# Optimization experiments

Hardware: AMD Instinct MI355X
Metric: run time of the kernel (lower is better)

## Reference

```python
import jax, jax.numpy as jnp
import numpy as np

N = 100000      # nodes
E = 1600000     # edges
IN, H, OUT = 128, 128, 64
FUSION_W = 0.5


def setup_inputs() -> dict:
    key = jax.random.key(0)
    ks = jax.random.split(key, 10)
    x = jax.random.normal(ks[0], (N, IN), dtype=jnp.float32)
    edge_index = jax.random.randint(ks[1], (2, E), 0, N, dtype=jnp.int32)

    def lin(k, fi, fo):
        return jax.random.normal(k, (fi, fo), dtype=jnp.float32) / np.float32(np.sqrt(fi))

    return {
        "x": x,
        "edge_index": edge_index,
        "gnn_W1": lin(ks[2], IN, H),  "gnn_b1": jnp.zeros((H,), jnp.float32),
        "gnn_W2": lin(ks[3], H, OUT), "gnn_b2": jnp.zeros((OUT,), jnp.float32),
        "mlp_W1": lin(ks[4], IN, H),  "mlp_b1": jnp.zeros((H,), jnp.float32),
        "mlp_W2": lin(ks[5], H, OUT), "mlp_b2": jnp.zeros((OUT,), jnp.float32),
    }


def _gcn_conv(x, W, b, src, dst, deg_inv_sqrt, deg_inv):
    # GCNConv: x' = D^{-1/2} (A + I) D^{-1/2} (x W) + b, deg counts self-loops
    h = x @ W                                     # [N, F_out]
    norm = deg_inv_sqrt[src] * deg_inv_sqrt[dst]  # [E]
    agg = jax.ops.segment_sum(h[src] * norm[:, None], dst, num_segments=N)
    # self-loop contribution has norm 1/deg
    return agg + h * deg_inv[:, None] + b


def reference(x, edge_index, gnn_W1, gnn_b1, gnn_W2, gnn_b2,
              mlp_W1, mlp_b1, mlp_W2, mlp_b2):
    src, dst = edge_index[0], edge_index[1]
    # in-degree including self-loops (PyG GCNConv default add_self_loops=True)
    deg = 1.0 + jax.ops.segment_sum(jnp.ones((E,), jnp.float32), dst, num_segments=N)
    deg_inv_sqrt = jax.lax.rsqrt(deg)
    deg_inv = 1.0 / deg

    # GNN branch (dropout is identity in eval mode)
    h = jax.nn.relu(_gcn_conv(x, gnn_W1, gnn_b1, src, dst, deg_inv_sqrt, deg_inv))
    z_gnn = _gcn_conv(h, gnn_W2, gnn_b2, src, dst, deg_inv_sqrt, deg_inv)

    # MLP branch
    z_mlp = jax.nn.relu(x @ mlp_W1 + mlp_b1) @ mlp_W2 + mlp_b2

    return FUSION_W * z_gnn + (1.0 - FUSION_W) * z_mlp
```

## Files before the change

### kernel.cpp

```cpp
#include <hip/hip_runtime.h>
#include <hip/hip_fp16.h>

static constexpr int IN_F = 128;
static constexpr int FCAP = 6144;

typedef _Float16 half8 __attribute__((ext_vector_type(8)));
typedef _Float16 half4 __attribute__((ext_vector_type(4)));
typedef float f32x4 __attribute__((ext_vector_type(4)));
typedef float f32x2 __attribute__((ext_vector_type(2)));

__device__ inline void fp8x8_to_f32(uint2 u, float* f) {
    f32x2 a0 = __builtin_amdgcn_cvt_pk_f32_fp8(u.x, false);
    f32x2 a1 = __builtin_amdgcn_cvt_pk_f32_fp8(u.x, true);
    f32x2 a2 = __builtin_amdgcn_cvt_pk_f32_fp8(u.y, false);
    f32x2 a3 = __builtin_amdgcn_cvt_pk_f32_fp8(u.y, true);
    f[0] = a0[0]; f[1] = a0[1]; f[2] = a1[0]; f[3] = a1[1];
    f[4] = a2[0]; f[5] = a2[1]; f[6] = a3[0]; f[7] = a3[1];
}
__device__ inline void fp8x4_to_f32(unsigned u, float* f) {
    f32x2 a0 = __builtin_amdgcn_cvt_pk_f32_fp8(u, false);
    f32x2 a1 = __builtin_amdgcn_cvt_pk_f32_fp8(u, true);
    f[0] = a0[0]; f[1] = a0[1]; f[2] = a1[0]; f[3] = a1[1];
}
__device__ inline unsigned char f32_to_fp8(float v) {
    return (unsigned char)__builtin_amdgcn_cvt_pk_fp8_f32(v, v, 0, false);
}


__global__ __launch_bounds__(1024) void kb_count(const int* __restrict__ dst,
                                                 int* __restrict__ bcount, int E) {
    __shared__ int cnt[512];
    const int tid = threadIdx.x;
    if (tid < 512) cnt[tid] = 0;
    __syncthreads();
#pragma unroll
    for (int q = 0; q < 8; ++q) {
        int i = blockIdx.x * 8192 + q * 1024 + tid;
        if (i < E) atomicAdd(&cnt[dst[i] >> 8], 1);
    }
    __syncthreads();
    if (tid < 512 && cnt[tid] > 0) atomicAdd(&bcount[tid], cnt[tid]);
}

__global__ __launch_bounds__(512) void k_scanb(const int* __restrict__ bcount,
                                               int* __restrict__ bbase,
                                               int* __restrict__ bcursor, int NB) {
    __shared__ int s[512];
    const int tid = threadIdx.x;
    int v = (tid < NB) ? bcount[tid] : 0;
    s[tid] = v;
    __syncthreads();
    int inc = v;
#pragma unroll
    for (int off = 1; off < 512; off <<= 1) {
        int add = (tid >= off) ? s[tid - off] : 0;
        __syncthreads();
        s[tid] = inc = inc + add;
        __syncthreads();
    }
    if (tid < NB) { bbase[tid] = inc - v; bcursor[tid] = inc - v; }
    if (tid == NB - 1) bbase[NB] = inc;
}

__global__ __launch_bounds__(1024) void kb_move(const int* __restrict__ src,
                                                const int* __restrict__ dst,
                                                int* __restrict__ bcursor,
                                                unsigned* __restrict__ recs, int E) {
    __shared__ int cnt[512];
    __shared__ int off[512];
    const int tid = threadIdx.x;
    if (tid < 512) cnt[tid] = 0;
    __syncthreads();

    int bq[8];
    unsigned rq[8];
#pragma unroll
    for (int q = 0; q < 8; ++q) {
        int i = blockIdx.x * 8192 + q * 1024 + tid;
        if (i < E) {
            int d = dst[i];
            int s = src[i];
            bq[q] = d >> 8;
            rq[q] = (unsigned)(((d & 255) << 17) | s);
            atomicAdd(&cnt[bq[q]], 1);
        } else {
            bq[q] = -1;
            rq[q] = 0u;
        }
    }
    __syncthreads();
    if (tid < 512 && cnt[tid] > 0) off[tid] = atomicAdd(&bcursor[tid], cnt[tid]);
    __syncthreads();
#pragma unroll
    for (int q = 0; q < 8; ++q) {
        if (bq[q] >= 0) {
            int p = atomicAdd(&off[bq[q]], 1);
            recs[p] = rq[q];
        }
    }
}

__global__ __launch_bounds__(256) void kb_fill_lds(const unsigned* __restrict__ recs,
                                                   const int* __restrict__ bbase,
                                                   int* __restrict__ row_ptr,
                                                   float* __restrict__ dis,
                                                   int* __restrict__ csr, int n) {
    __shared__ int hist[256];
    __shared__ int sc[256];
    __shared__ int base[257];
    __shared__ int cur[256];
    __shared__ int stage[FCAP];
    const int tid   = threadIdx.x;
    const int b     = blockIdx.x;
    const int s     = bbase[b], e = bbase[b + 1];
    const int nbase = b << 8;

    hist[tid] = 0;
    __syncthreads();
    for (int i = s + tid; i < e; i += 256)
        atomicAdd(&hist[recs[i] >> 17], 1);
    __syncthreads();

    const int v = hist[tid];
    sc[tid] = v;
    __syncthreads();
    int inc = v;
#pragma unroll
    for (int off = 1; off < 256; off <<= 1) {
        int add = (tid >= off) ? sc[tid - off] : 0;
        __syncthreads();
        sc[tid] = inc = inc + add;
        __syncthreads();
    }
    const int excl = inc - v;
    base[tid] = excl;
    if (tid == 255) base[256] = inc;
    cur[tid] = 0;

    const int idx = nbase + tid;
    if (idx < n) {
        row_ptr[idx] = s + excl;
        dis[idx] = rsqrtf(1.0f + (float)v);
    }
    if (idx == n) row_ptr[n] = s + excl;
    if (tid == 255 && nbase + 256 == n) row_ptr[n] = s + inc;
    __syncthreads();

    for (int i = s + tid; i < e; i += 256) {
        unsigned r = recs[i];
        int dl = (int)(r >> 17);
        int slot = base[dl] + atomicAdd(&cur[dl], 1);
        int sr = (int)(r & 0x1FFFFu);
        if (slot < FCAP) stage[slot] = sr;
        else csr[s + slot] = sr;
    }
    __syncthreads();

    const int total = e - s;
    const int lim = total < FCAP ? total : FCAP;
    for (int i = tid; i < lim; i += 256)
        csr[s + i] = stage[i];
}

__global__ __launch_bounds__(256) void k_prep_w(const float* __restrict__ gW1,
                                                const float* __restrict__ mW1,
                                                const float* __restrict__ mW2,
                                                const float* __restrict__ gW2,
                                                _Float16* __restrict__ tg1,
                                                _Float16* __restrict__ tm1,
                                                _Float16* __restrict__ tm2,
                                                _Float16* __restrict__ tg2) {
    int i = blockIdx.x * 256 + threadIdx.x;
    if (i < 16384)      { int j = i;         int f = j >> 7, k = j & 127; tg1[j] = (_Float16)gW1[k * 128 + f]; }
    else if (i < 32768) { int j = i - 16384; int f = j >> 7, k = j & 127; tm1[j] = (_Float16)mW1[k * 128 + f]; }
    else if (i < 40960) { int j = i - 32768; int f = j >> 7, k = j & 127; tm2[j] = (_Float16)mW2[k * 64 + f]; }
    else if (i < 49152) { int j = i - 40960; int f = j >> 7, k = j & 127; tg2[j] = (_Float16)gW2[k * 64 + f]; }
}

__global__ __launch_bounds__(256) void k_dual_mfma(const float* __restrict__ x,
                                                   const _Float16* __restrict__ tg1,
                                                   const _Float16* __restrict__ tm1,
                                                   const _Float16* __restrict__ tm2,
                                                   const float* __restrict__ b1,
                                                   const float* __restrict__ b2,
                                                   const float* __restrict__ dis,
                                                   unsigned char* __restrict__ h1,
                                                   _Float16* __restrict__ z, int nrows) {
    __shared__ _Float16 As[64 * 128];
    __shared__ _Float16 Ws[128 * 128];
    _Float16* Ms = As;
    const int tid  = threadIdx.x;
    const int row0 = blockIdx.x * 64;

#pragma unroll
    for (int p = 0; p < 4; ++p) {
        int sid = p * 256 + tid;
        int r = sid >> 4, s = sid & 15;
        int gr = row0 + r;
        uint4 v = make_uint4(0, 0, 0, 0);
        if (gr < nrows) {
            const float4 f0 = *reinterpret_cast<const float4*>(x + (size_t)gr * 128 + s * 8);
            const float4 f1 = *reinterpret_cast<const float4*>(x + (size_t)gr * 128 + s * 8 + 4);
            _Float16 t[8] = {(_Float16)f0.x, (_Float16)f0.y, (_Float16)f0.z, (_Float16)f0.w,
                             (_Float16)f1.x, (_Float16)f1.y, (_Float16)f1.z, (_Float16)f1.w};
            v = *reinterpret_cast<uint4*>(t);
        }
        *reinterpret_cast<uint4*>(&As[r * 128 + ((s ^ (r & 7)) * 8)]) = v;
    }
#pragma unroll
    for (int p = 0; p < 8; ++p) {
        int sid = p * 256 + tid;
        int r = sid >> 4, s = sid & 15;
        uint4 v = *reinterpret_cast<const uint4*>(tg1 + (size_t)r * 128 + s * 8);
        *reinterpret_cast<uint4*>(&Ws[r * 128 + ((s ^ (r & 7)) * 8)]) = v;
    }
    __syncthreads();

    const int lane = tid & 63;
    const int wv   = tid >> 6;
    const int mrow = wv * 16 + (lane & 15);
    const int kg   = lane >> 4;
    const int grow = row0 + wv * 16 + kg * 4;

    half8 a[4];
#pragma unroll
    for (int kk = 0; kk < 4; ++kk)
        a[kk] = *reinterpret_cast<const half8*>(&As[mrow * 128 + (((kk * 4 + kg) ^ (mrow & 7)) * 8)]);

    float dvals[4];
#pragma unroll
    for (int j = 0; j < 4; ++j)
        dvals[j] = (grow + j < nrows) ? dis[grow + j] : 0.f;

#pragma unroll
    for (int ct = 0; ct < 8; ++ct) {
        const int ncol = ct * 16 + (lane & 15);
        f32x4 acc = {0.f, 0.f, 0.f, 0.f};
#pragma unroll
        for (int kk = 0; kk < 4; ++kk) {
            half8 b = *reinterpret_cast<const half8*>(&Ws[ncol * 128 + (((kk * 4 + kg) ^ (ncol & 7)) * 8)]);
            acc = __builtin_amdgcn_mfma_f32_16x16x32_f16(a[kk], b, acc, 0, 0, 0);
        }
#pragma unroll
        for (int j = 0; j < 4; ++j)
            if (grow + j < nrows)
                h1[(size_t)(grow + j) * 128 + ncol] = f32_to_fp8(acc[j] * dvals[j]);
    }
    __syncthreads();

#pragma unroll
    for (int p = 0; p < 8; ++p) {
        int sid = p * 256 + tid;
        int r = sid >> 4, s = sid & 15;
        uint4 v = *reinterpret_cast<const uint4*>(tm1 + (size_t)r * 128 + s * 8);
        *reinterpret_cast<uint4*>(&Ws[r * 128 + ((s ^ (r & 7)) * 8)]) = v;
    }
    __syncthreads();

#pragma unroll
    for (int ct = 0; ct < 8; ++ct) {
        const int ncol = ct * 16 + (lane & 15);
        f32x4 acc = {0.f, 0.f, 0.f, 0.f};
#pragma unroll
        for (int kk = 0; kk < 4; ++kk) {
            half8 b = *reinterpret_cast<const half8*>(&Ws[ncol * 128 + (((kk * 4 + kg) ^ (ncol & 7)) * 8)]);
            acc = __builtin_amdgcn_mfma_f32_16x16x32_f16(a[kk], b, acc, 0, 0, 0);
        }
        const float bias = b1[ncol];
#pragma unroll
        for (int j = 0; j < 4; ++j) {
            int r = wv * 16 + kg * 4 + j;
            float v = fmaxf((float)acc[j] + bias, 0.f);
            Ms[r * 128 + (((ncol >> 3) ^ (r & 7)) * 8) + (ncol & 7)] = (_Float16)v;
        }
    }
    __syncthreads();

#pragma unroll
    for (int p = 0; p < 4; ++p) {
        int sid = p * 256 + tid;
        int r = sid >> 4, s = sid & 15;
        uint4 v = *reinterpret_cast<const uint4*>(tm2 + (size_t)r * 128 + s * 8);
        *reinterpret_cast<uint4*>(&Ws[r * 128 + ((s ^ (r & 7)) * 8)]) = v;
    }
    __syncthreads();

    half8 am[4];
#pragma unroll
    for (int kk = 0; kk < 4; ++kk)
        am[kk] = *reinterpret_cast<const half8*>(&Ms[mrow * 128 + (((kk * 4 + kg) ^ (mrow & 7)) * 8)]);

#pragma unroll
    for (int ct = 0; ct < 4; ++ct) {
        const int ncol = ct * 16 + (lane & 15);
        f32x4 acc = {0.f, 0.f, 0.f, 0.f};
#pragma unroll
        for (int kk = 0; kk < 4; ++kk) {
            half8 b = *reinterpret_cast<const half8*>(&Ws[ncol * 128 + (((kk * 4 + kg) ^ (ncol & 7)) * 8)]);
            acc = __builtin_amdgcn_mfma_f32_16x16x32_f16(am[kk], b, acc, 0, 0, 0);
        }
        const float bias = b2[ncol];
#pragma unroll
        for (int j = 0; j < 4; ++j)
            if (grow + j < nrows)
                z[(size_t)(grow + j) * 64 + ncol] = (_Float16)((float)acc[j] + bias);
    }
}

__global__ __launch_bounds__(256) void k_mm64(const _Float16* __restrict__ A,
                                              const _Float16* __restrict__ Wt,
                                              const float* __restrict__ dis,
                                              unsigned char* __restrict__ C, int nrows) {
    __shared__ _Float16 As[64 * 128];
    __shared__ _Float16 Ws[64 * 128];
    const int tid  = threadIdx.x;
    const int row0 = blockIdx.x * 64;

#pragma unroll
    for (int p = 0; p < 4; ++p) {
        int sid = p * 256 + tid;
        int r = sid >> 4, s = sid & 15;
        int gr = row0 + r;
        uint4 v = make_uint4(0, 0, 0, 0);
        if (gr < nrows) v = *reinterpret_cast<const uint4*>(A + (size_t)gr * 128 + s * 8);
        *reinterpret_cast<uint4*>(&As[r * 128 + ((s ^ (r & 7)) * 8)]) = v;
    }
#pragma unroll
    for (int p = 0; p < 4; ++p) {
        int sid = p * 256 + tid;
        int r = sid >> 4, s = sid & 15;
        uint4 v = *reinterpret_cast<const uint4*>(Wt + (size_t)r * 128 + s * 8);
        *reinterpret_cast<uint4*>(&Ws[r * 128 + ((s ^ (r & 7)) * 8)]) = v;
    }
    __syncthreads();

    const int lane = tid & 63;
    const int wv   = tid >> 6;
    const int mrow = wv * 16 + (lane & 15);
    const int kg   = lane >> 4;
    const int grow = row0 + wv * 16 + kg * 4;

    half8 a[4];
#pragma unroll
    for (int kk = 0; kk < 4; ++kk)
        a[kk] = *reinterpret_cast<const half8*>(&As[mrow * 128 + (((kk * 4 + kg) ^ (mrow & 7)) * 8)]);

    float dvals[4];
#pragma unroll
    for (int j = 0; j < 4; ++j)
        dvals[j] = (grow + j < nrows) ? dis[grow + j] : 0.f;

#pragma unroll
    for (int ct = 0; ct < 4; ++ct) {
        const int ncol = ct * 16 + (lane & 15);
        f32x4 acc = {0.f, 0.f, 0.f, 0.f};
#pragma unroll
        for (int kk = 0; kk < 4; ++kk) {
            half8 b = *reinterpret_cast<const half8*>(&Ws[ncol * 128 + (((kk * 4 + kg) ^ (ncol & 7)) * 8)]);
            acc = __builtin_amdgcn_mfma_f32_16x16x32_f16(a[kk], b, acc, 0, 0, 0);
        }
#pragma unroll
        for (int j = 0; j < 4; ++j)
            if (grow + j < nrows)
                C[(size_t)(grow + j) * 64 + ncol] = f32_to_fp8(acc[j] * dvals[j]);
    }
}

__global__ __launch_bounds__(256) void k_agg1(const int* __restrict__ rp,
                                              const int* __restrict__ csr,
                                              const float* __restrict__ dis,
                                              const unsigned char* __restrict__ h1,
                                              const float* __restrict__ b,
                                              _Float16* __restrict__ out, int n) {
    const int tid  = threadIdx.x;
    const int node = blockIdx.x * 4 + (tid >> 6);
    if (node >= n) return;
    const int lane = tid & 63;
    const int g    = lane >> 4;
    const int c0   = (lane & 15) * 8;
    const int start = rp[node], end = rp[node + 1];

    float acc[8];
#pragma unroll
    for (int k = 0; k < 8; ++k) acc[k] = 0.f;

    int j = start + g;
    for (; j + 12 < end; j += 16) {
        int s0 = csr[j];
        int s1 = csr[j + 4];
        int s2 = csr[j + 8];
        int s3 = csr[j + 12];
        uint2 u0 = *reinterpret_cast<const uint2*>(h1 + (size_t)s0 * 128 + c0);
        uint2 u1 = *reinterpret_cast<const uint2*>(h1 + (size_t)s1 * 128 + c0);
        uint2 u2 = *reinterpret_cast<const uint2*>(h1 + (size_t)s2 * 128 + c0);
        uint2 u3 = *reinterpret_cast<const uint2*>(h1 + (size_t)s3 * 128 + c0);
        float f0[8], f1[8], f2[8], f3[8];
        fp8x8_to_f32(u0, f0);
        fp8x8_to_f32(u1, f1);
        fp8x8_to_f32(u2, f2);
        fp8x8_to_f32(u3, f3);
#pragma unroll
        for (int k = 0; k < 8; ++k)
            acc[k] += (f0[k] + f1[k]) + (f2[k] + f3[k]);
    }
    for (; j < end; j += 4) {
        int s0 = csr[j];
        uint2 u0 = *reinterpret_cast<const uint2*>(h1 + (size_t)s0 * 128 + c0);
        float f0[8];
        fp8x8_to_f32(u0, f0);
#pragma unroll
        for (int k = 0; k < 8; ++k) acc[k] += f0[k];
    }

#pragma unroll
    for (int k = 0; k < 8; ++k) {
        acc[k] += __shfl_xor(acc[k], 16);
        acc[k] += __shfl_xor(acc[k], 32);
    }

    if (g == 0) {
        const float dd = dis[node];
        uint2 un = *reinterpret_cast<const uint2*>(h1 + (size_t)node * 128 + c0);
        float fn[8];
        fp8x8_to_f32(un, fn);
        const float4 bv0 = *reinterpret_cast<const float4*>(b + c0);
        const float4 bv1 = *reinterpret_cast<const float4*>(b + c0 + 4);
        const float bb[8] = {bv0.x, bv0.y, bv0.z, bv0.w, bv1.x, bv1.y, bv1.z, bv1.w};
        half8 o;
#pragma unroll
        for (int k = 0; k < 8; ++k)
            o[k] = (_Float16)fmaxf(dd * (acc[k] + fn[k]) + bb[k], 0.f);
        *reinterpret_cast<half8*>(out + (size_t)node * 128 + c0) = o;
    }
}

__global__ __launch_bounds__(256) void k_agg2(const int* __restrict__ rp,
                                              const int* __restrict__ csr,
                                              const float* __restrict__ dis,
                                              const unsigned char* __restrict__ h2,
                                              const float* __restrict__ b,
                                              const _Float16* __restrict__ zmlp,
                                              float* __restrict__ out, int n) {
    const int tid  = threadIdx.x;
    const int node = blockIdx.x * 4 + (tid >> 6);
    if (node >= n) return;
    const int lane = tid & 63;
    const int g    = lane >> 4;
    const int c0   = (lane & 15) * 4;
    const int start = rp[node], end = rp[node + 1];

    float acc[4];
#pragma unroll
    for (int k = 0; k < 4; ++k) acc[k] = 0.f;

    int j = start + g;
    for (; j + 12 < end; j += 16) {
        int s0 = csr[j];
        int s1 = csr[j + 4];
        int s2 = csr[j + 8];
        int s3 = csr[j + 12];
        unsigned u0 = *reinterpret_cast<const unsigned*>(h2 + (size_t)s0 * 64 + c0);
        unsigned u1 = *reinterpret_cast<const unsigned*>(h2 + (size_t)s1 * 64 + c0);
        unsigned u2 = *reinterpret_cast<const unsigned*>(h2 + (size_t)s2 * 64 + c0);
        unsigned u3 = *reinterpret_cast<const unsigned*>(h2 + (size_t)s3 * 64 + c0);
        float f0[4], f1[4], f2[4], f3[4];
        fp8x4_to_f32(u0, f0);
        fp8x4_to_f32(u1, f1);
        fp8x4_to_f32(u2, f2);
        fp8x4_to_f32(u3, f3);
#pragma unroll
        for (int k = 0; k < 4; ++k)
            acc[k] += (f0[k] + f1[k]) + (f2[k] + f3[k]);
    }
    for (; j < end; j += 4) {
        int s0 = csr[j];
        unsigned u0 = *reinterpret_cast<const unsigned*>(h2 + (size_t)s0 * 64 + c0);
        float f0[4];
        fp8x4_to_f32(u0, f0);
#pragma unroll
        for (int k = 0; k < 4; ++k) acc[k] += f0[k];
    }

#pragma unroll
    for (int k = 0; k < 4; ++k) {
        acc[k] += __shfl_xor(acc[k], 16);
        acc[k] += __shfl_xor(acc[k], 32);
    }

    if (g == 0) {
        const float dd = dis[node];
        unsigned un = *reinterpret_cast<const unsigned*>(h2 + (size_t)node * 64 + c0);
        float fn[4];
        fp8x4_to_f32(un, fn);
        half4 zm = *reinterpret_cast<const half4*>(zmlp + (size_t)node * 64 + c0);
        const float4 bv = *reinterpret_cast<const float4*>(b + c0);
        const float bb[4] = {bv.x, bv.y, bv.z, bv.w};
        float4 o;
        float* op = &o.x;
#pragma unroll
        for (int k = 0; k < 4; ++k)
            op[k] = 0.5f * ((dd * (acc[k] + fn[k]) + bb[k]) + (float)zm[k]);
        *reinterpret_cast<float4*>(out + (size_t)node * 64 + c0) = o;
    }
}

extern "C" void kernel_launch(void* const* d_in, const int* in_sizes, int n_in,
                              void* d_out, int out_size, void* d_ws, size_t ws_size,
                              hipStream_t stream) {
    const float* x      = (const float*)d_in[0];
    const int* edge_idx = (const int*)d_in[1];
    const float* gnn_W1 = (const float*)d_in[2];
    const float* gnn_b1 = (const float*)d_in[3];
    const float* gnn_W2 = (const float*)d_in[4];
    const float* gnn_b2 = (const float*)d_in[5];
    const float* mlp_W1 = (const float*)d_in[6];
    const float* mlp_b1 = (const float*)d_in[7];
    const float* mlp_W2 = (const float*)d_in[8];
    const float* mlp_b2 = (const float*)d_in[9];
    float* out = (float*)d_out;

    const int N = in_sizes[0] / IN_F;
    const int E = in_sizes[1] / 2;
    const int* src = edge_idx;
    const int* dst = edge_idx + E;

    const int NB = (N + 255) >> 8;

    char* wp = (char*)d_ws;
    int* row_ptr   = (int*)wp;            wp += ((size_t)N + 4) * sizeof(int);
    int* bbase     = (int*)wp;            wp += 516 * sizeof(int);
    int* bcursor   = (int*)wp;            wp += 512 * sizeof(int);
    int* bcount    = (int*)wp;            wp += 512 * sizeof(int);
    int* csr       = (int*)wp;            wp += (size_t)E * sizeof(int);
    unsigned* recs = (unsigned*)wp;       wp += (size_t)E * sizeof(unsigned);
    float* dis     = (float*)wp;          wp += (size_t)N * sizeof(float);
    _Float16* tg1  = (_Float16*)wp;       wp += 16384 * sizeof(_Float16);
    _Float16* tm1  = (_Float16*)wp;       wp += 16384 * sizeof(_Float16);
    _Float16* tm2  = (_Float16*)wp;       wp += 8192 * sizeof(_Float16);
    _Float16* tg2  = (_Float16*)wp;       wp += 8192 * sizeof(_Float16);
    unsigned char* h1 = (unsigned char*)wp;  wp += (size_t)N * 128;
    _Float16* hmid = (_Float16*)wp;       wp += (size_t)N * 128 * sizeof(_Float16);
    unsigned char* h2 = (unsigned char*)wp;  wp += (size_t)N * 64;
    wp = (char*)(((uintptr_t)wp + 15) & ~(uintptr_t)15);
    _Float16* zmlp = (_Float16*)wp;       wp += (size_t)N * 64 * sizeof(_Float16);

    k_prep_w<<<192, 256, 0, stream>>>(gnn_W1, mlp_W1, mlp_W2, gnn_W2, tg1, tm1, tm2, tg2);

    hipMemsetAsync(bcount, 0, 512 * sizeof(int), stream);
    const int mvblocks = (E + 8191) / 8192;
    kb_count<<<mvblocks, 1024, 0, stream>>>(dst, bcount, E);
    k_scanb<<<1, 512, 0, stream>>>(bcount, bbase, bcursor, NB);
    kb_move<<<mvblocks, 1024, 0, stream>>>(src, dst, bcursor, recs, E);
    kb_fill_lds<<<NB, 256, 0, stream>>>(recs, bbase, row_ptr, dis, csr, N);

    const int gblocks = (N + 63) / 64;

    k_dual_mfma<<<gblocks, 256, 0, stream>>>(x, tg1, tm1, tm2, mlp_b1, mlp_b2, dis, h1, zmlp, N);

    k_agg1<<<(N + 3) / 4, 256, 0, stream>>>(row_ptr, csr, dis, h1, gnn_b1, hmid, N);

    k_mm64<<<gblocks, 256, 0, stream>>>(hmid, tg2, dis, h2, N);

    k_agg2<<<(N + 3) / 4, 256, 0, stream>>>(row_ptr, csr, dis, h2, gnn_b2, zmlp, out, N);
}
```

Before: 212.5 us.

## Privatize LDS bucket histograms per wave, read weights from global, pack fp8 accumulation

```diff
diff --git a/kernel.cpp b/kernel.cpp
--- a/kernel.cpp
+++ b/kernel.cpp
@@ -9,6 +9,16 @@
 typedef float f32x4 __attribute__((ext_vector_type(4)));
 typedef float f32x2 __attribute__((ext_vector_type(2)));
 
+__device__ inline void acc_fp8x8(uint2 u, f32x2* a) {
+    a[0] += __builtin_amdgcn_cvt_pk_f32_fp8(u.x, false);
+    a[1] += __builtin_amdgcn_cvt_pk_f32_fp8(u.x, true);
+    a[2] += __builtin_amdgcn_cvt_pk_f32_fp8(u.y, false);
+    a[3] += __builtin_amdgcn_cvt_pk_f32_fp8(u.y, true);
+}
+__device__ inline void acc_fp8x4(unsigned u, f32x2* a) {
+    a[0] += __builtin_amdgcn_cvt_pk_f32_fp8(u, false);
+    a[1] += __builtin_amdgcn_cvt_pk_f32_fp8(u, true);
+}
 __device__ inline void fp8x8_to_f32(uint2 u, float* f) {
     f32x2 a0 = __builtin_amdgcn_cvt_pk_f32_fp8(u.x, false);
     f32x2 a1 = __builtin_amdgcn_cvt_pk_f32_fp8(u.x, true);
@@ -29,17 +39,23 @@
 
 __global__ __launch_bounds__(1024) void kb_count(const int* __restrict__ dst,
                                                  int* __restrict__ bcount, int E) {
-    __shared__ int cnt[512];
+    __shared__ int cnt[16][512];
     const int tid = threadIdx.x;
-    if (tid < 512) cnt[tid] = 0;
+    const int wv  = tid >> 6;
+    for (int i = tid; i < 16 * 512; i += 1024) (&cnt[0][0])[i] = 0;
     __syncthreads();
 #pragma unroll
     for (int q = 0; q < 8; ++q) {
         int i = blockIdx.x * 8192 + q * 1024 + tid;
-        if (i < E) atomicAdd(&cnt[dst[i] >> 8], 1);
-    }
-    __syncthreads();
-    if (tid < 512 && cnt[tid] > 0) atomicAdd(&bcount[tid], cnt[tid]);
+        if (i < E) atomicAdd(&cnt[wv][dst[i] >> 8], 1);
+    }
+    __syncthreads();
+    if (tid < 512) {
+        int run = 0;
+#pragma unroll
+        for (int w = 0; w < 16; ++w) run += cnt[w][tid];
+        if (run > 0) atomicAdd(&bcount[tid], run);
+    }
 }
 
 __global__ __launch_bounds__(512) void k_scanb(const int* __restrict__ bcount,
@@ -66,10 +82,11 @@
                                                 const int* __restrict__ dst,
                                                 int* __restrict__ bcursor,
                                                 unsigned* __restrict__ recs, int E) {
-    __shared__ int cnt[512];
-    __shared__ int off[512];
+    __shared__ int cnt[16][512];
+    __shared__ int gbase[512];
     const int tid = threadIdx.x;
-    if (tid < 512) cnt[tid] = 0;
+    const int wv  = tid >> 6;
+    for (int i = tid; i < 16 * 512; i += 1024) (&cnt[0][0])[i] = 0;
     __syncthreads();
 
     int bq[8];
@@ -82,25 +99,34 @@
             int s = src[i];
             bq[q] = d >> 8;
             rq[q] = (unsigned)(((d & 255) << 17) | s);
-            atomicAdd(&cnt[bq[q]], 1);
+            atomicAdd(&cnt[wv][bq[q]], 1);
         } else {
             bq[q] = -1;
             rq[q] = 0u;
         }
     }
     __syncthreads();
-    if (tid < 512 && cnt[tid] > 0) off[tid] = atomicAdd(&bcursor[tid], cnt[tid]);
+    if (tid < 512) {
+        int run = 0;
+#pragma unroll
+        for (int w = 0; w < 16; ++w) {
+            int t = cnt[w][tid];
+            cnt[w][tid] = run;
+            run += t;
+        }
+        gbase[tid] = (run > 0) ? atomicAdd(&bcursor[tid], run) : 0;
+    }
     __syncthreads();
 #pragma unroll
     for (int q = 0; q < 8; ++q) {
         if (bq[q] >= 0) {
-            int p = atomicAdd(&off[bq[q]], 1);
+            int p = gbase[bq[q]] + atomicAdd(&cnt[wv][bq[q]], 1);
             recs[p] = rq[q];
         }
     }
 }
 
-__global__ __launch_bounds__(256) void kb_fill_lds(const unsigned* __restrict__ recs,
+__global__ __launch_bounds__(512) void kb_fill_lds(const unsigned* __restrict__ recs,
                                                    const int* __restrict__ bbase,
                                                    int* __restrict__ row_ptr,
                                                    float* __restrict__ dis,
@@ -115,38 +141,40 @@
     const int s     = bbase[b], e = bbase[b + 1];
     const int nbase = b << 8;
 
-    hist[tid] = 0;
-    __syncthreads();
-    for (int i = s + tid; i < e; i += 256)
+    if (tid < 256) hist[tid] = 0;
+    __syncthreads();
+    for (int i = s + tid; i < e; i += 512)
         atomicAdd(&hist[recs[i] >> 17], 1);
     __syncthreads();
 
-    const int v = hist[tid];
-    sc[tid] = v;
+    const int v = (tid < 256) ? hist[tid] : 0;
+    if (tid < 256) sc[tid] = v;
     __syncthreads();
     int inc = v;
 #pragma unroll
     for (int off = 1; off < 256; off <<= 1) {
-        int add = (tid >= off) ? sc[tid - off] : 0;
+        int add = (tid >= off && tid < 256) ? sc[tid - off] : 0;
         __syncthreads();
-        sc[tid] = inc = inc + add;
+        if (tid < 256) sc[tid] = inc = inc + add;
         __syncthreads();
     }
-    const int excl = inc - v;
-    base[tid] = excl;
-    if (tid == 255) base[256] = inc;
-    cur[tid] = 0;
-
-    const int idx = nbase + tid;
-    if (idx < n) {
-        row_ptr[idx] = s + excl;
-        dis[idx] = rsqrtf(1.0f + (float)v);
-    }
-    if (idx == n) row_ptr[n] = s + excl;
-    if (tid == 255 && nbase + 256 == n) row_ptr[n] = s + inc;
-    __syncthreads();
-
-    for (int i = s + tid; i < e; i += 256) {
+    if (tid < 256) {
+        const int excl = inc - v;
+        base[tid] = excl;
+        if (tid == 255) base[256] = inc;
+        cur[tid] = 0;
+
+        const int idx = nbase + tid;
+        if (idx < n) {
+            row_ptr[idx] = s + excl;
+            dis[idx] = rsqrtf(1.0f + (float)v);
+        }
+        if (idx == n) row_ptr[n] = s + excl;
+        if (tid == 255 && nbase + 256 == n) row_ptr[n] = s + inc;
+    }
+    __syncthreads();
+
+    for (int i = s + tid; i < e; i += 512) {
         unsigned r = recs[i];
         int dl = (int)(r >> 17);
         int slot = base[dl] + atomicAdd(&cur[dl], 1);
@@ -158,7 +186,7 @@
 
     const int total = e - s;
     const int lim = total < FCAP ? total : FCAP;
-    for (int i = tid; i < lim; i += 256)
+    for (int i = tid; i < lim; i += 512)
         csr[s + i] = stage[i];
 }
 
@@ -187,7 +215,6 @@
                                                    unsigned char* __restrict__ h1,
                                                    _Float16* __restrict__ z, int nrows) {
     __shared__ _Float16 As[64 * 128];
-    __shared__ _Float16 Ws[128 * 128];
     _Float16* Ms = As;
     const int tid  = threadIdx.x;
     const int row0 = blockIdx.x * 64;
@@ -207,13 +234,6 @@
         }
         *reinterpret_cast<uint4*>(&As[r * 128 + ((s ^ (r & 7)) * 8)]) = v;
     }
-#pragma unroll
-    for (int p = 0; p < 8; ++p) {
-        int sid = p * 256 + tid;
-        int r = sid >> 4, s = sid & 15;
-        uint4 v = *reinterpret_cast<const uint4*>(tg1 + (size_t)r * 128 + s * 8);
-        *reinterpret_cast<uint4*>(&Ws[r * 128 + ((s ^ (r & 7)) * 8)]) = v;
-    }
     __syncthreads();
 
     const int lane = tid & 63;
@@ -238,7 +258,7 @@
         f32x4 acc = {0.f, 0.f, 0.f, 0.f};
 #pragma unroll
         for (int kk = 0; kk < 4; ++kk) {
-            half8 b = *reinterpret_cast<const half8*>(&Ws[ncol * 128 + (((kk * 4 + kg) ^ (ncol & 7)) * 8)]);
+            half8 b = *reinterpret_cast<const half8*>(tg1 + (size_t)ncol * 128 + (kk * 4 + kg) * 8);
             acc = __builtin_amdgcn_mfma_f32_16x16x32_f16(a[kk], b, acc, 0, 0, 0);
         }
 #pragma unroll
@@ -249,21 +269,12 @@
     __syncthreads();
 
 #pragma unroll
-    for (int p = 0; p < 8; ++p) {
-        int sid = p * 256 + tid;
-        int r = sid >> 4, s = sid & 15;
-        uint4 v = *reinterpret_cast<const uint4*>(tm1 + (size_t)r * 128 + s * 8);
-        *reinterpret_cast<uint4*>(&Ws[r * 128 + ((s ^ (r & 7)) * 8)]) = v;
-    }
-    __syncthreads();
-
-#pragma unroll
     for (int ct = 0; ct < 8; ++ct) {
         const int ncol = ct * 16 + (lane & 15);
         f32x4 acc = {0.f, 0.f, 0.f, 0.f};
 #pragma unroll
         for (int kk = 0; kk < 4; ++kk) {
-            half8 b = *reinterpret_cast<const half8*>(&Ws[ncol * 128 + (((kk * 4 + kg) ^ (ncol & 7)) * 8)]);
+            half8 b = *reinterpret_cast<const half8*>(tm1 + (size_t)ncol * 128 + (kk * 4 + kg) * 8);
             acc = __builtin_amdgcn_mfma_f32_16x16x32_f16(a[kk], b, acc, 0, 0, 0);
         }
         const float bias = b1[ncol];
@@ -276,15 +287,6 @@
     }
     __syncthreads();
 
-#pragma unroll
-    for (int p = 0; p < 4; ++p) {
-        int sid = p * 256 + tid;
-        int r = sid >> 4, s = sid & 15;
-        uint4 v = *reinterpret_cast<const uint4*>(tm2 + (size_t)r * 128 + s * 8);
-        *reinterpret_cast<uint4*>(&Ws[r * 128 + ((s ^ (r & 7)) * 8)]) = v;
-    }
-    __syncthreads();
-
     half8 am[4];
 #pragma unroll
     for (int kk = 0; kk < 4; ++kk)
@@ -296,7 +298,7 @@
         f32x4 acc = {0.f, 0.f, 0.f, 0.f};
 #pragma unroll
         for (int kk = 0; kk < 4; ++kk) {
-            half8 b = *reinterpret_cast<const half8*>(&Ws[ncol * 128 + (((kk * 4 + kg) ^ (ncol & 7)) * 8)]);
+            half8 b = *reinterpret_cast<const half8*>(tm2 + (size_t)ncol * 128 + (kk * 4 + kg) * 8);
             acc = __builtin_amdgcn_mfma_f32_16x16x32_f16(am[kk], b, acc, 0, 0, 0);
         }
         const float bias = b2[ncol];
@@ -312,7 +314,6 @@
                                               const float* __restrict__ dis,
                                               unsigned char* __restrict__ C, int nrows) {
     __shared__ _Float16 As[64 * 128];
-    __shared__ _Float16 Ws[64 * 128];
     const int tid  = threadIdx.x;
     const int row0 = blockIdx.x * 64;
 
@@ -325,13 +326,6 @@
         if (gr < nrows) v = *reinterpret_cast<const uint4*>(A + (size_t)gr * 128 + s * 8);
         *reinterpret_cast<uint4*>(&As[r * 128 + ((s ^ (r & 7)) * 8)]) = v;
     }
-#pragma unroll
-    for (int p = 0; p < 4; ++p) {
-        int sid = p * 256 + tid;
-        int r = sid >> 4, s = sid & 15;
-        uint4 v = *reinterpret_cast<const uint4*>(Wt + (size_t)r * 128 + s * 8);
-        *reinterpret_cast<uint4*>(&Ws[r * 128 + ((s ^ (r & 7)) * 8)]) = v;
-    }
     __syncthreads();
 
     const int lane = tid & 63;
@@ -356,7 +350,7 @@
         f32x4 acc = {0.f, 0.f, 0.f, 0.f};
 #pragma unroll
         for (int kk = 0; kk < 4; ++kk) {
-            half8 b = *reinterpret_cast<const half8*>(&Ws[ncol * 128 + (((kk * 4 + kg) ^ (ncol & 7)) * 8)]);
+            half8 b = *reinterpret_cast<const half8*>(Wt + (size_t)ncol * 128 + (kk * 4 + kg) * 8);
             acc = __builtin_amdgcn_mfma_f32_16x16x32_f16(a[kk], b, acc, 0, 0, 0);
         }
 #pragma unroll
@@ -380,9 +374,7 @@
     const int c0   = (lane & 15) * 8;
     const int start = rp[node], end = rp[node + 1];
 
-    float acc[8];
-#pragma unroll
-    for (int k = 0; k < 8; ++k) acc[k] = 0.f;
+    f32x2 acc[4] = {{0.f, 0.f}, {0.f, 0.f}, {0.f, 0.f}, {0.f, 0.f}};
 
     int j = start + g;
     for (; j + 12 < end; j += 16) {
@@ -394,28 +386,23 @@
         uint2 u1 = *reinterpret_cast<const uint2*>(h1 + (size_t)s1 * 128 + c0);
         uint2 u2 = *reinterpret_cast<const uint2*>(h1 + (size_t)s2 * 128 + c0);
         uint2 u3 = *reinterpret_cast<const uint2*>(h1 + (size_t)s3 * 128 + c0);
-        float f0[8], f1[8], f2[8], f3[8];
-        fp8x8_to_f32(u0, f0);
-        fp8x8_to_f32(u1, f1);
-        fp8x8_to_f32(u2, f2);
-        fp8x8_to_f32(u3, f3);
-#pragma unroll
-        for (int k = 0; k < 8; ++k)
-            acc[k] += (f0[k] + f1[k]) + (f2[k] + f3[k]);
+        acc_fp8x8(u0, acc);
+        acc_fp8x8(u1, acc);
+        acc_fp8x8(u2, acc);
+        acc_fp8x8(u3, acc);
     }
     for (; j < end; j += 4) {
         int s0 = csr[j];
         uint2 u0 = *reinterpret_cast<const uint2*>(h1 + (size_t)s0 * 128 + c0);
-        float f0[8];
-        fp8x8_to_f32(u0, f0);
-#pragma unroll
-        for (int k = 0; k < 8; ++k) acc[k] += f0[k];
-    }
-
+        acc_fp8x8(u0, acc);
+    }
+
+    float av[8] = {acc[0][0], acc[0][1], acc[1][0], acc[1][1],
+                   acc[2][0], acc[2][1], acc[3][0], acc[3][1]};
 #pragma unroll
     for (int k = 0; k < 8; ++k) {
-        acc[k] += __shfl_xor(acc[k], 16);
-        acc[k] += __shfl_xor(acc[k], 32);
+        av[k] += __shfl_xor(av[k], 16);
+        av[k] += __shfl_xor(av[k], 32);
     }
 
     if (g == 0) {
@@ -429,7 +416,7 @@
         half8 o;
 #pragma unroll
         for (int k = 0; k < 8; ++k)
-            o[k] = (_Float16)fmaxf(dd * (acc[k] + fn[k]) + bb[k], 0.f);
+            o[k] = (_Float16)fmaxf(dd * (av[k] + fn[k]) + bb[k], 0.f);
         *reinterpret_cast<half8*>(out + (size_t)node * 128 + c0) = o;
     }
 }
@@ -449,9 +436,7 @@
     const int c0   = (lane & 15) * 4;
     const int start = rp[node], end = rp[node + 1];
 
-    float acc[4];
-#pragma unroll
-    for (int k = 0; k < 4; ++k) acc[k] = 0.f;
+    f32x2 acc[2] = {{0.f, 0.f}, {0.f, 0.f}};
 
     int j = start + g;
     for (; j + 12 < end; j += 16) {
@@ -463,28 +448,22 @@
         unsigned u1 = *reinterpret_cast<const unsigned*>(h2 + (size_t)s1 * 64 + c0);
         unsigned u2 = *reinterpret_cast<const unsigned*>(h2 + (size_t)s2 * 64 + c0);
         unsigned u3 = *reinterpret_cast<const unsigned*>(h2 + (size_t)s3 * 64 + c0);
-        float f0[4], f1[4], f2[4], f3[4];
-        fp8x4_to_f32(u0, f0);
-        fp8x4_to_f32(u1, f1);
-        fp8x4_to_f32(u2, f2);
-        fp8x4_to_f32(u3, f3);
-#pragma unroll
-        for (int k = 0; k < 4; ++k)
-            acc[k] += (f0[k] + f1[k]) + (f2[k] + f3[k]);
+        acc_fp8x4(u0, acc);
+        acc_fp8x4(u1, acc);
+        acc_fp8x4(u2, acc);
+        acc_fp8x4(u3, acc);
     }
     for (; j < end; j += 4) {
         int s0 = csr[j];
         unsigned u0 = *reinterpret_cast<const unsigned*>(h2 + (size_t)s0 * 64 + c0);
-        float f0[4];
-        fp8x4_to_f32(u0, f0);
-#pragma unroll
-        for (int k = 0; k < 4; ++k) acc[k] += f0[k];
-    }
-
+        acc_fp8x4(u0, acc);
+    }
+
+    float av[4] = {acc[0][0], acc[0][1], acc[1][0], acc[1][1]};
 #pragma unroll
     for (int k = 0; k < 4; ++k) {
-        acc[k] += __shfl_xor(acc[k], 16);
-        acc[k] += __shfl_xor(acc[k], 32);
+        av[k] += __shfl_xor(av[k], 16);
+        av[k] += __shfl_xor(av[k], 32);
     }
 
     if (g == 0) {
@@ -499,7 +478,7 @@
         float* op = &o.x;
 #pragma unroll
         for (int k = 0; k < 4; ++k)
-            op[k] = 0.5f * ((dd * (acc[k] + fn[k]) + bb[k]) + (float)zm[k]);
+            op[k] = 0.5f * ((dd * (av[k] + fn[k]) + bb[k]) + (float)zm[k]);
         *reinterpret_cast<float4*>(out + (size_t)node * 64 + c0) = o;
     }
 }
@@ -551,7 +530,7 @@
     kb_count<<<mvblocks, 1024, 0, stream>>>(dst, bcount, E);
     k_scanb<<<1, 512, 0, stream>>>(bcount, bbase, bcursor, NB);
     kb_move<<<mvblocks, 1024, 0, stream>>>(src, dst, bcursor, recs, E);
-    kb_fill_lds<<<NB, 256, 0, stream>>>(recs, bbase, row_ptr, dis, csr, N);
+    kb_fill_lds<<<NB, 512, 0, stream>>>(recs, bbase, row_ptr, dis, csr, N);
 
     const int gblocks = (N + 63) / 64;
 
```

Result: slower. 247.7 us (+16.6%).
